# Performance work log

Hardware: AMD Instinct MI355X
Metric: run time of the kernel (lower is better)

The kernel has to match this reference:

```python
import jax, jax.numpy as jnp
import numpy as np

N = 50000
E = 800000


def spmm(edge_index, edge_weight, x, n):
    # sparse (n,n) @ dense (n,d) via gather + segment_sum
    rows, cols = edge_index[0], edge_index[1]
    return jax.ops.segment_sum(edge_weight[:, None] * x[cols], rows, num_segments=n)


def setup_inputs() -> dict:
    key = jax.random.key(0)
    ks = jax.random.split(key, 12)
    return {
        "omics1": jax.random.normal(ks[0], (N, 2000), dtype=jnp.float32),
        "omics2": jax.random.normal(ks[1], (N, 500), dtype=jnp.float32),
        "edge_index1": jax.random.randint(ks[2], (2, E), 0, N, dtype=jnp.int32),
        "edge_weight1": jax.random.uniform(ks[3], (E,), dtype=jnp.float32),
        "edge_index2": jax.random.randint(ks[4], (2, E), 0, N, dtype=jnp.int32),
        "edge_weight2": jax.random.uniform(ks[5], (E,), dtype=jnp.float32),
        "W_enc1": jax.random.normal(ks[6], (2000, 64), dtype=jnp.float32) * 0.03,
        "W_enc2": jax.random.normal(ks[7], (500, 64), dtype=jnp.float32) * 0.06,
        "w_omega": jax.random.normal(ks[8], (64, 64), dtype=jnp.float32) * 0.12,
        "u_omega": jax.random.normal(ks[9], (64, 1), dtype=jnp.float32) * 0.17,
        "W_dec1": jax.random.normal(ks[10], (64, 2000), dtype=jnp.float32) * 0.12,
        "W_dec2": jax.random.normal(ks[11], (64, 500), dtype=jnp.float32) * 0.12,
    }


def reference(omics1, omics2, edge_index1, edge_weight1, edge_index2, edge_weight2,
              W_enc1, W_enc2, w_omega, u_omega, W_dec1, W_dec2):
    n = omics1.shape[0]
    # encoder GCNs (act=None per Encoder_omics default)
    e1 = spmm(edge_index1, edge_weight1, omics1 @ W_enc1, n)  # (N,64)
    e2 = spmm(edge_index2, edge_weight2, omics2 @ W_enc2, n)  # (N,64)
    # attention fusion across modalities
    emb = jnp.stack([e1, e2], axis=1)                 # (N,2,64)
    v = jnp.tanh(emb @ w_omega)                       # (N,2,64)
    vu = jnp.squeeze(v @ u_omega, -1)                 # (N,2)
    alpha = jax.nn.softmax(vu, axis=1)                # (N,2)
    emb_combined = jnp.sum(emb * alpha[..., None], axis=1)  # (N,64)
    # decoder GCNs
    d1 = spmm(edge_index1, edge_weight1, emb_combined @ W_dec1, n)  # (N,2000)
    d2 = spmm(edge_index2, edge_weight2, emb_combined @ W_dec2, n)  # (N,500)
    return (e1, e2, emb_combined, alpha, d1, d2)
```

## Files before the change

### kernel.cpp

```cpp
#include <hip/hip_runtime.h>
#include <math.h>

#define NN 50000
#define NE 800000
#define IPSET 1563
#define NITEMS (2 * IPSET)
#define SLOTS 64

typedef __attribute__((ext_vector_type(8))) short bf16x8;
typedef __attribute__((ext_vector_type(4))) float f32x4;

__device__ __forceinline__ ushort f2bf(float f) {
    union { float f; unsigned u; } v; v.f = f;
    unsigned r = v.u + 0x7FFFu + ((v.u >> 16) & 1u);
    return (ushort)(r >> 16);
}

__device__ __forceinline__ float bf2f(ushort u) {
    union { unsigned u; float f; } v; v.u = ((unsigned)u) << 16;
    return v.f;
}

__device__ __forceinline__ void frag_one(const float* __restrict__ src, ushort* __restrict__ dst,
                                         int K, int Nc, int t) {
    int nct = (Nc + 15) >> 4;
    int lane = t & 63, rest = t >> 6;
    int ct = rest % nct, g = rest / nct;
    int col = ct * 16 + (lane & 15);
    int kb = g * 32 + (lane >> 4) * 8;
    ushort u[8];
    #pragma unroll
    for (int j = 0; j < 8; ++j) {
        int k = kb + j;
        float v = (k < K && col < Nc) ? src[(size_t)k * Nc + col] : 0.f;
        u[j] = f2bf(v);
    }
    *(bf16x8*)&dst[(size_t)t * 8] = *(bf16x8*)u;
}

__global__ __launch_bounds__(256) void frag_zero(
    const float* __restrict__ s0, ushort* __restrict__ d0, int K0, int N0, int n0,
    const float* __restrict__ s1, ushort* __restrict__ d1, int K1, int N1, int n1,
    const float* __restrict__ s2, ushort* __restrict__ d2, int K2, int N2, int n2,
    const float* __restrict__ s3, ushort* __restrict__ d3, int K3, int N3, int n3,
    int* __restrict__ zbuf, int nz) {
    int t = blockIdx.x * 256 + threadIdx.x;
    if (t < n0) { frag_one(s0, d0, K0, N0, t); return; } t -= n0;
    if (t < n1) { frag_one(s1, d1, K1, N1, t); return; } t -= n1;
    if (t < n2) { frag_one(s2, d2, K2, N2, t); return; } t -= n2;
    if (t < n3) { frag_one(s3, d3, K3, N3, t); return; } t -= n3;
    if (t < nz) zbuf[t] = 0;
}

__device__ __forceinline__ void enc_item(
    const float* __restrict__ A, const ushort* __restrict__ Bf, ushort* __restrict__ C,
    int K, int item, int lane) {
    const int M = NN;
    const int klo = (lane >> 4) * 8;
    int r0 = item * 32 + (lane & 15);
    int r1 = r0 + 16;
    const float* ap0 = A + (size_t)(r0 < M ? r0 : M - 1) * K;
    const float* ap1 = A + (size_t)(r1 < M ? r1 : M - 1) * K;
    const bf16x8* bv = (const bf16x8*)Bf;
    const int ng = (K + 31) >> 5;
    f32x4 acc[2][4] = {};
    #pragma unroll 2
    for (int g = 0; g < ng; ++g) {
        int kg = g * 32 + klo;
        bf16x8 af[2];
        #pragma unroll
        for (int tt = 0; tt < 2; ++tt) {
            const float* ap = tt ? ap1 : ap0;
            float v[8];
            if (kg + 7 < K) {
                f32x4 a = *(const f32x4*)(ap + kg);
                f32x4 b = *(const f32x4*)(ap + kg + 4);
                v[0] = a.x; v[1] = a.y; v[2] = a.z; v[3] = a.w;
                v[4] = b.x; v[5] = b.y; v[6] = b.z; v[7] = b.w;
            } else {
                #pragma unroll
                for (int j = 0; j < 8; ++j) v[j] = (kg + j < K) ? ap[kg + j] : 0.f;
            }
            ushort u[8];
            #pragma unroll
            for (int j = 0; j < 8; ++j) u[j] = f2bf(v[j]);
            af[tt] = *(bf16x8*)u;
        }
        #pragma unroll
        for (int ct = 0; ct < 4; ++ct) {
            bf16x8 b = bv[(g * 4 + ct) * 64 + lane];
            acc[0][ct] = __builtin_amdgcn_mfma_f32_16x16x32_bf16(b, af[0], acc[0][ct], 0, 0, 0);
            acc[1][ct] = __builtin_amdgcn_mfma_f32_16x16x32_bf16(b, af[1], acc[1][ct], 0, 0, 0);
        }
    }
    const int cq = (lane >> 4) * 4;
    #pragma unroll
    for (int tt = 0; tt < 2; ++tt) {
        int row = item * 32 + tt * 16 + (lane & 15);
        if (row < M) {
            #pragma unroll
            for (int ct = 0; ct < 4; ++ct) {
                ushort u4[4] = { f2bf(acc[tt][ct][0]), f2bf(acc[tt][ct][1]),
                                 f2bf(acc[tt][ct][2]), f2bf(acc[tt][ct][3]) };
                *(ushort4*)&C[(size_t)row * 64 + ct * 16 + cq] = *(ushort4*)u4;
            }
        }
    }
}

__global__ __launch_bounds__(256) void k1_bucket_enc(
    const int* __restrict__ r1, const int* __restrict__ ce1, const float* __restrict__ w1,
    int* __restrict__ cnt1, int2* __restrict__ buf1,
    const int* __restrict__ r2, const int* __restrict__ ce2, const float* __restrict__ w2,
    int* __restrict__ cnt2, int2* __restrict__ buf2, int nsb,
    const float* __restrict__ A1, const ushort* __restrict__ Bf1, ushort* __restrict__ C1, int K1,
    const float* __restrict__ A2, const ushort* __restrict__ Bf2, ushort* __restrict__ C2, int K2) {
    if ((int)blockIdx.x < nsb) {
        int stride = nsb * 256;
        for (int i = blockIdx.x * 256 + threadIdx.x; i < 2 * NE; i += stride) {
            if (i < NE) {
                int r = r1[i];
                int s = atomicAdd(&cnt1[r], 1);
                if (s < SLOTS) buf1[(size_t)r * SLOTS + s] = make_int2(ce1[i], __float_as_int(w1[i]));
            } else {
                int j = i - NE;
                int r = r2[j];
                int s = atomicAdd(&cnt2[r], 1);
                if (s < SLOTS) buf2[(size_t)r * SLOTS + s] = make_int2(ce2[j], __float_as_int(w2[j]));
            }
        }
        return;
    }
    int item = (blockIdx.x - nsb) * 4 + (threadIdx.x >> 6);
    if (item < NITEMS) {
        int lane = threadIdx.x & 63;
        if (item < IPSET) enc_item(A1, Bf1, C1, K1, item, lane);
        else              enc_item(A2, Bf2, C2, K2, item - IPSET, lane);
    }
}

__device__ __forceinline__ void spmm_row2(
    const int2* __restrict__ p1, int n1, const ushort* __restrict__ x1,
    const int2* __restrict__ p2, int n2, const ushort* __restrict__ x2,
    int lane, float& acc1o, float& acc2o) {
    float acc1 = 0.f, acc2 = 0.f;
    int i1 = 0, i2 = 0;
    while (i1 + 3 < n1 && i2 + 3 < n2) {
        int2 a0 = p1[i1], a1 = p1[i1 + 1], a2 = p1[i1 + 2], a3 = p1[i1 + 3];
        int2 b0 = p2[i2], b1 = p2[i2 + 1], b2 = p2[i2 + 2], b3 = p2[i2 + 3];
        float ga0 = bf2f(x1[(size_t)a0.x * 64 + lane]);
        float gb0 = bf2f(x2[(size_t)b0.x * 64 + lane]);
        float ga1 = bf2f(x1[(size_t)a1.x * 64 + lane]);
        float gb1 = bf2f(x2[(size_t)b1.x * 64 + lane]);
        float ga2 = bf2f(x1[(size_t)a2.x * 64 + lane]);
        float gb2 = bf2f(x2[(size_t)b2.x * 64 + lane]);
        float ga3 = bf2f(x1[(size_t)a3.x * 64 + lane]);
        float gb3 = bf2f(x2[(size_t)b3.x * 64 + lane]);
        acc1 += __int_as_float(a0.y) * ga0; acc2 += __int_as_float(b0.y) * gb0;
        acc1 += __int_as_float(a1.y) * ga1; acc2 += __int_as_float(b1.y) * gb1;
        acc1 += __int_as_float(a2.y) * ga2; acc2 += __int_as_float(b2.y) * gb2;
        acc1 += __int_as_float(a3.y) * ga3; acc2 += __int_as_float(b3.y) * gb3;
        i1 += 4; i2 += 4;
    }
    for (; i1 + 3 < n1; i1 += 4) {
        int2 a0 = p1[i1], a1 = p1[i1 + 1], a2 = p1[i1 + 2], a3 = p1[i1 + 3];
        float g0 = bf2f(x1[(size_t)a0.x * 64 + lane]);
        float g1 = bf2f(x1[(size_t)a1.x * 64 + lane]);
        float g2 = bf2f(x1[(size_t)a2.x * 64 + lane]);
        float g3 = bf2f(x1[(size_t)a3.x * 64 + lane]);
        acc1 += __int_as_float(a0.y) * g0; acc1 += __int_as_float(a1.y) * g1;
        acc1 += __int_as_float(a2.y) * g2; acc1 += __int_as_float(a3.y) * g3;
    }
    for (; i2 + 3 < n2; i2 += 4) {
        int2 b0 = p2[i2], b1 = p2[i2 + 1], b2 = p2[i2 + 2], b3 = p2[i2 + 3];
        float g0 = bf2f(x2[(size_t)b0.x * 64 + lane]);
        float g1 = bf2f(x2[(size_t)b1.x * 64 + lane]);
        float g2 = bf2f(x2[(size_t)b2.x * 64 + lane]);
        float g3 = bf2f(x2[(size_t)b3.x * 64 + lane]);
        acc2 += __int_as_float(b0.y) * g0; acc2 += __int_as_float(b1.y) * g1;
        acc2 += __int_as_float(b2.y) * g2; acc2 += __int_as_float(b3.y) * g3;
    }
    for (; i1 < n1; ++i1) {
        int2 p = p1[i1];
        acc1 += __int_as_float(p.y) * bf2f(x1[(size_t)p.x * 64 + lane]);
    }
    for (; i2 < n2; ++i2) {
        int2 p = p2[i2];
        acc2 += __int_as_float(p.y) * bf2f(x2[(size_t)p.x * 64 + lane]);
    }
    acc1o = acc1; acc2o = acc2;
}

__global__ __launch_bounds__(256) void spmm_attn(
    const int* __restrict__ cnt1, const int2* __restrict__ buf1, const ushort* __restrict__ x1,
    const int* __restrict__ cnt2, const int2* __restrict__ buf2, const ushort* __restrict__ x2,
    const float* __restrict__ Wo, const float* __restrict__ uo,
    float* __restrict__ e1, float* __restrict__ e2,
    float* __restrict__ emb, ushort* __restrict__ embb, float* __restrict__ alpha) {
    const int lane = threadIdx.x & 63;
    const int node = (blockIdx.x * 256 + threadIdx.x) >> 6;
    if (node >= NN) return;

    int n1 = cnt1[node]; if (n1 > SLOTS) n1 = SLOTS;
    int n2 = cnt2[node]; if (n2 > SLOTS) n2 = SLOTS;
    float ev0, ev1;
    spmm_row2(buf1 + (size_t)node * SLOTS, n1, x1,
              buf2 + (size_t)node * SLOTS, n2, x2, lane, ev0, ev1);

    float acc1 = 0.f, acc2 = 0.f;
    #pragma unroll 8
    for (int k = 0; k < 64; ++k) {
        float wv = Wo[k * 64 + lane];
        acc1 = fmaf(__shfl(ev0, k), wv, acc1);
        acc2 = fmaf(__shfl(ev1, k), wv, acc2);
    }
    float u = uo[lane];
    float t1 = tanhf(acc1) * u;
    float t2 = tanhf(acc2) * u;
    #pragma unroll
    for (int off = 32; off; off >>= 1) {
        t1 += __shfl_xor(t1, off);
        t2 += __shfl_xor(t2, off);
    }
    float m = fmaxf(t1, t2);
    float a1 = expf(t1 - m), a2 = expf(t2 - m);
    float sden = a1 + a2;
    a1 /= sden; a2 /= sden;

    const size_t base = (size_t)node * 64;
    float ec = a1 * ev0 + a2 * ev1;
    e1[base + lane] = ev0;
    e2[base + lane] = ev1;
    emb[base + lane] = ec;
    embb[base + lane] = f2bf(ec);
    if (lane == 0) *(float2*)&alpha[(size_t)node * 2] = make_float2(a1, a2);
}

__global__ __launch_bounds__(256) void spmm_dec(
    const int* __restrict__ cnt1, const int2* __restrict__ buf1,
    const int* __restrict__ cnt2, const int2* __restrict__ buf2,
    const ushort* __restrict__ xb, ushort* __restrict__ s1b, ushort* __restrict__ s2b) {
    const int lane = threadIdx.x & 63;
    const int row = (blockIdx.x * 256 + threadIdx.x) >> 6;
    if (row >= NN) return;
    int n1 = cnt1[row]; if (n1 > SLOTS) n1 = SLOTS;
    int n2 = cnt2[row]; if (n2 > SLOTS) n2 = SLOTS;
    float acc1, acc2;
    spmm_row2(buf1 + (size_t)row * SLOTS, n1, xb,
              buf2 + (size_t)row * SLOTS, n2, xb, lane, acc1, acc2);
    s1b[(size_t)row * 64 + lane] = f2bf(acc1);
    s2b[(size_t)row * 64 + lane] = f2bf(acc2);
}

__device__ __forceinline__ void dec_item(
    const ushort* __restrict__ S, const ushort* __restrict__ Wf, float* __restrict__ C,
    int Nc, int nct, int item, int lane) {
    const int M = NN;
    const int klo = (lane >> 4) * 8;
    int r0 = item * 32 + (lane & 15);
    int r1 = r0 + 16;
    const ushort* sp0 = S + (size_t)(r0 < M ? r0 : M - 1) * 64;
    const ushort* sp1 = S + (size_t)(r1 < M ? r1 : M - 1) * 64;
    bf16x8 af00 = *(const bf16x8*)(sp0 + klo);
    bf16x8 af01 = *(const bf16x8*)(sp0 + 32 + klo);
    bf16x8 af10 = *(const bf16x8*)(sp1 + klo);
    bf16x8 af11 = *(const bf16x8*)(sp1 + 32 + klo);
    const bf16x8* wv = (const bf16x8*)Wf;
    const int row0 = item * 32 + (lane & 15);
    const int cq = (lane >> 4) * 4;
    #pragma unroll 2
    for (int ct = 0; ct < nct; ++ct) {
        bf16x8 w0 = wv[ct * 64 + lane];
        bf16x8 w1 = wv[(nct + ct) * 64 + lane];
        f32x4 acc0 = {}, acc1 = {};
        acc0 = __builtin_amdgcn_mfma_f32_16x16x32_bf16(w0, af00, acc0, 0, 0, 0);
        acc0 = __builtin_amdgcn_mfma_f32_16x16x32_bf16(w1, af01, acc0, 0, 0, 0);
        acc1 = __builtin_amdgcn_mfma_f32_16x16x32_bf16(w0, af10, acc1, 0, 0, 0);
        acc1 = __builtin_amdgcn_mfma_f32_16x16x32_bf16(w1, af11, acc1, 0, 0, 0);
        int colbase = ct * 16 + cq;
        if (colbase + 3 < Nc) {
            if (row0 < M)      *(f32x4*)&C[(size_t)row0 * Nc + colbase] = acc0;
            if (row0 + 16 < M) *(f32x4*)&C[(size_t)(row0 + 16) * Nc + colbase] = acc1;
        }
    }
}

__global__ __launch_bounds__(256) void gemm_dec4(
    const ushort* __restrict__ S1, const ushort* __restrict__ Wf1, float* __restrict__ C1, int Nc1, int nct1,
    const ushort* __restrict__ S2, const ushort* __restrict__ Wf2, float* __restrict__ C2, int Nc2, int nct2) {
    int item = blockIdx.x * 4 + (threadIdx.x >> 6);
    if (item >= NITEMS) return;
    const int lane = threadIdx.x & 63;
    if (item < IPSET) dec_item(S1, Wf1, C1, Nc1, nct1, item, lane);
    else              dec_item(S2, Wf2, C2, Nc2, nct2, item - IPSET, lane);
}

extern "C" void kernel_launch(void* const* d_in, const int* in_sizes, int n_in,
                              void* d_out, int out_size, void* d_ws, size_t ws_size,
                              hipStream_t stream) {
    const float* omics1 = (const float*)d_in[0];
    const float* omics2 = (const float*)d_in[1];
    const int*   ei1    = (const int*)d_in[2];
    const float* ew1    = (const float*)d_in[3];
    const int*   ei2    = (const int*)d_in[4];
    const float* ew2    = (const float*)d_in[5];
    const float* Wenc1  = (const float*)d_in[6];
    const float* Wenc2  = (const float*)d_in[7];
    const float* womega = (const float*)d_in[8];
    const float* uomega = (const float*)d_in[9];
    const float* Wdec1  = (const float*)d_in[10];
    const float* Wdec2  = (const float*)d_in[11];

    float* out  = (float*)d_out;
    float* e1   = out;
    float* e2   = e1 + (size_t)NN * 64;
    float* emb  = e2 + (size_t)NN * 64;
    float* alph = emb + (size_t)NN * 64;
    float* d1   = alph + (size_t)NN * 2;
    float* d2   = d1 + (size_t)NN * 2000;

    int2* buf1 = (int2*)d1;
    int2* buf2 = buf1 + (size_t)NN * SLOTS;

    const int nBf1 = 63 * 4 * 64;
    const int nBf2 = 16 * 4 * 64;
    const int nWf1 = 2 * 125 * 64;
    const int nWf2 = 2 * 32 * 64;

    char* w = (char*)d_ws;
    ushort* h1b = (ushort*)w;              w += (size_t)NN * 64 * 2;
    ushort* h2b = (ushort*)w;              w += (size_t)NN * 64 * 2;
    ushort* embb = (ushort*)w;             w += (size_t)NN * 64 * 2;
    ushort* s1b = (ushort*)w;              w += (size_t)NN * 64 * 2;
    ushort* s2b = (ushort*)w;              w += (size_t)NN * 64 * 2;
    int*   cnt1 = (int*)w;                 w += (size_t)NN * 4;
    int*   cnt2 = (int*)w;                 w += (size_t)NN * 4;
    ushort* Bf1 = (ushort*)w;              w += (size_t)nBf1 * 8 * 2;
    ushort* Bf2 = (ushort*)w;              w += (size_t)nBf2 * 8 * 2;
    ushort* Wf1 = (ushort*)w;              w += (size_t)nWf1 * 8 * 2;
    ushort* Wf2 = (ushort*)w;              w += (size_t)nWf2 * 8 * 2;

    dim3 b256(256);

    const int nz = 2 * NN;
    const int nfrag = nBf1 + nBf2 + nWf1 + nWf2 + nz;
    frag_zero<<<dim3((nfrag + 255) / 256), b256, 0, stream>>>(
        Wenc1, Bf1, 2000, 64, nBf1,
        Wenc2, Bf2, 500, 64, nBf2,
        Wdec1, Wf1, 64, 2000, nWf1,
        Wdec2, Wf2, 64, 500, nWf2,
        cnt1, nz);

    const int NSB = 512;
    k1_bucket_enc<<<dim3(NSB + (NITEMS + 3) / 4), b256, 0, stream>>>(
        ei1, ei1 + NE, ew1, cnt1, buf1,
        ei2, ei2 + NE, ew2, cnt2, buf2, NSB,
        omics1, Bf1, h1b, 2000, omics2, Bf2, h2b, 500);

    spmm_attn<<<dim3((NN + 3) / 4), b256, 0, stream>>>(
        cnt1, buf1, h1b, cnt2, buf2, h2b, womega, uomega, e1, e2, emb, embb, alph);

    spmm_dec<<<dim3((NN + 3) / 4), b256, 0, stream>>>(
        cnt1, buf1, cnt2, buf2, embb, s1b, s2b);

    gemm_dec4<<<dim3((NITEMS + 3) / 4), b256, 0, stream>>>(
        s1b, Wf1, d1, 2000, 125, s2b, Wf2, d2, 500, 32);
}
```

Measured before the change: 559.2 us.

## Fuse decoder-1 SpMM with its GEMM via LDS and use packed bf16 converts

```diff
diff --git a/kernel.cpp b/kernel.cpp
--- a/kernel.cpp
+++ b/kernel.cpp
@@ -19,6 +19,21 @@
 __device__ __forceinline__ float bf2f(ushort u) {
     union { unsigned u; float f; } v; v.u = ((unsigned)u) << 16;
     return v.f;
+}
+
+__device__ __forceinline__ unsigned cvtpk(float lo, float hi) {
+    unsigned r;
+    asm("v_cvt_pk_bf16_f32 %0, %1, %2" : "=v"(r) : "v"(lo), "v"(hi));
+    return r;
+}
+
+__device__ __forceinline__ bf16x8 cvt8pk(const float* v) {
+    union { unsigned u[4]; bf16x8 b; } o;
+    o.u[0] = cvtpk(v[0], v[1]);
+    o.u[1] = cvtpk(v[2], v[3]);
+    o.u[2] = cvtpk(v[4], v[5]);
+    o.u[3] = cvtpk(v[6], v[7]);
+    return o.b;
 }
 
 __device__ __forceinline__ void frag_one(const float* __restrict__ src, ushort* __restrict__ dst,
@@ -81,10 +96,7 @@
                 #pragma unroll
                 for (int j = 0; j < 8; ++j) v[j] = (kg + j < K) ? ap[kg + j] : 0.f;
             }
-            ushort u[8];
-            #pragma unroll
-            for (int j = 0; j < 8; ++j) u[j] = f2bf(v[j]);
-            af[tt] = *(bf16x8*)u;
+            af[tt] = cvt8pk(v);
         }
         #pragma unroll
         for (int ct = 0; ct < 4; ++ct) {
@@ -100,9 +112,10 @@
         if (row < M) {
             #pragma unroll
             for (int ct = 0; ct < 4; ++ct) {
-                ushort u4[4] = { f2bf(acc[tt][ct][0]), f2bf(acc[tt][ct][1]),
-                                 f2bf(acc[tt][ct][2]), f2bf(acc[tt][ct][3]) };
-                *(ushort4*)&C[(size_t)row * 64 + ct * 16 + cq] = *(ushort4*)u4;
+                uint2 uu;
+                uu.x = cvtpk(acc[tt][ct][0], acc[tt][ct][1]);
+                uu.y = cvtpk(acc[tt][ct][2], acc[tt][ct][3]);
+                *(uint2*)&C[(size_t)row * 64 + ct * 16 + cq] = uu;
             }
         }
     }
@@ -236,20 +249,54 @@
     if (lane == 0) *(float2*)&alpha[(size_t)node * 2] = make_float2(a1, a2);
 }
 
-__global__ __launch_bounds__(256) void spmm_dec(
+__global__ __launch_bounds__(256) void fused_dec1(
     const int* __restrict__ cnt1, const int2* __restrict__ buf1,
     const int* __restrict__ cnt2, const int2* __restrict__ buf2,
-    const ushort* __restrict__ xb, ushort* __restrict__ s1b, ushort* __restrict__ s2b) {
+    const ushort* __restrict__ xb, ushort* __restrict__ s2b,
+    const ushort* __restrict__ Wf1, float* __restrict__ C1) {
+    __shared__ ushort sm1[32 * 64];
     const int lane = threadIdx.x & 63;
-    const int row = (blockIdx.x * 256 + threadIdx.x) >> 6;
-    if (row >= NN) return;
-    int n1 = cnt1[row]; if (n1 > SLOTS) n1 = SLOTS;
-    int n2 = cnt2[row]; if (n2 > SLOTS) n2 = SLOTS;
-    float acc1, acc2;
-    spmm_row2(buf1 + (size_t)row * SLOTS, n1, xb,
-              buf2 + (size_t)row * SLOTS, n2, xb, lane, acc1, acc2);
-    s1b[(size_t)row * 64 + lane] = f2bf(acc1);
-    s2b[(size_t)row * 64 + lane] = f2bf(acc2);
+    const int wvid = threadIdx.x >> 6;
+    const int rbase = blockIdx.x * 32;
+
+    #pragma unroll 1
+    for (int j = 0; j < 8; ++j) {
+        int lr = wvid * 8 + j;
+        int row = rbase + lr;
+        float a1 = 0.f, a2 = 0.f;
+        if (row < NN) {
+            int n1 = cnt1[row]; if (n1 > SLOTS) n1 = SLOTS;
+            int n2 = cnt2[row]; if (n2 > SLOTS) n2 = SLOTS;
+            spmm_row2(buf1 + (size_t)row * SLOTS, n1, xb,
+                      buf2 + (size_t)row * SLOTS, n2, xb, lane, a1, a2);
+            s2b[(size_t)row * 64 + lane] = f2bf(a2);
+        }
+        sm1[lr * 64 + (lane ^ ((lr & 7) << 3))] = f2bf(a1);
+    }
+    __syncthreads();
+
+    const int klo = (lane >> 4) * 8;
+    const int r0 = lane & 15;
+    const int r1 = r0 + 16;
+    bf16x8 af00 = *(const bf16x8*)&sm1[r0 * 64 + (klo ^ ((r0 & 7) << 3))];
+    bf16x8 af01 = *(const bf16x8*)&sm1[r0 * 64 + ((32 + klo) ^ ((r0 & 7) << 3))];
+    bf16x8 af10 = *(const bf16x8*)&sm1[r1 * 64 + (klo ^ ((r1 & 7) << 3))];
+    bf16x8 af11 = *(const bf16x8*)&sm1[r1 * 64 + ((32 + klo) ^ ((r1 & 7) << 3))];
+    const bf16x8* wvp = (const bf16x8*)Wf1;
+    const int row0 = rbase + r0;
+    const int cq = (lane >> 4) * 4;
+    for (int ct = wvid; ct < 125; ct += 4) {
+        bf16x8 w0 = wvp[ct * 64 + lane];
+        bf16x8 w1 = wvp[(125 + ct) * 64 + lane];
+        f32x4 accA = {}, accB = {};
+        accA = __builtin_amdgcn_mfma_f32_16x16x32_bf16(w0, af00, accA, 0, 0, 0);
+        accA = __builtin_amdgcn_mfma_f32_16x16x32_bf16(w1, af01, accA, 0, 0, 0);
+        accB = __builtin_amdgcn_mfma_f32_16x16x32_bf16(w0, af10, accB, 0, 0, 0);
+        accB = __builtin_amdgcn_mfma_f32_16x16x32_bf16(w1, af11, accB, 0, 0, 0);
+        int colbase = ct * 16 + cq;
+        if (row0 < NN)      *(f32x4*)&C1[(size_t)row0 * 2000 + colbase] = accA;
+        if (row0 + 16 < NN) *(f32x4*)&C1[(size_t)(row0 + 16) * 2000 + colbase] = accB;
+    }
 }
 
 __device__ __forceinline__ void dec_item(
@@ -285,14 +332,10 @@
     }
 }
 
-__global__ __launch_bounds__(256) void gemm_dec4(
-    const ushort* __restrict__ S1, const ushort* __restrict__ Wf1, float* __restrict__ C1, int Nc1, int nct1,
-    const ushort* __restrict__ S2, const ushort* __restrict__ Wf2, float* __restrict__ C2, int Nc2, int nct2) {
+__global__ __launch_bounds__(256) void gemm_d2(
+    const ushort* __restrict__ s2b, const ushort* __restrict__ Wf2, float* __restrict__ C2) {
     int item = blockIdx.x * 4 + (threadIdx.x >> 6);
-    if (item >= NITEMS) return;
-    const int lane = threadIdx.x & 63;
-    if (item < IPSET) dec_item(S1, Wf1, C1, Nc1, nct1, item, lane);
-    else              dec_item(S2, Wf2, C2, Nc2, nct2, item - IPSET, lane);
+    if (item < IPSET) dec_item(s2b, Wf2, C2, 500, 32, item, threadIdx.x & 63);
 }
 
 extern "C" void kernel_launch(void* const* d_in, const int* in_sizes, int n_in,
@@ -319,7 +362,7 @@
     float* d1   = alph + (size_t)NN * 2;
     float* d2   = d1 + (size_t)NN * 2000;
 
-    int2* buf1 = (int2*)d1;
+    int2* buf1 = (int2*)d2;
     int2* buf2 = buf1 + (size_t)NN * SLOTS;
 
     const int nBf1 = 63 * 4 * 64;
@@ -331,7 +374,6 @@
     ushort* h1b = (ushort*)w;              w += (size_t)NN * 64 * 2;
     ushort* h2b = (ushort*)w;              w += (size_t)NN * 64 * 2;
     ushort* embb = (ushort*)w;             w += (size_t)NN * 64 * 2;
-    ushort* s1b = (ushort*)w;              w += (size_t)NN * 64 * 2;
     ushort* s2b = (ushort*)w;              w += (size_t)NN * 64 * 2;
     int*   cnt1 = (int*)w;                 w += (size_t)NN * 4;
     int*   cnt2 = (int*)w;                 w += (size_t)NN * 4;
@@ -360,9 +402,8 @@
     spmm_attn<<<dim3((NN + 3) / 4), b256, 0, stream>>>(
         cnt1, buf1, h1b, cnt2, buf2, h2b, womega, uomega, e1, e2, emb, embb, alph);
 
-    spmm_dec<<<dim3((NN + 3) / 4), b256, 0, stream>>>(
-        cnt1, buf1, cnt2, buf2, embb, s1b, s2b);
-
-    gemm_dec4<<<dim3((NITEMS + 3) / 4), b256, 0, stream>>>(
-        s1b, Wf1, d1, 2000, 125, s2b, Wf2, d2, 500, 32);
-}
+    fused_dec1<<<dim3(IPSET), b256, 0, stream>>>(
+        cnt1, buf1, cnt2, buf2, embb, s2b, Wf1, d1);
+
+    gemm_d2<<<dim3((IPSET + 3) / 4), b256, 0, stream>>>(s2b, Wf2, d2);
+}
```

After: 613.7 us. 9.7% more time.
